# Kernel optimization log

Measured on AMD Instinct MI355X. Metric: run time of the kernel, lower is better.

The kernel has to match this reference:

```python
import jax, jax.numpy as jnp
import numpy as np

OUT = 12                # out_size (cubic grid)
V = OUT * OUT * OUT     # voxels per roi


def setup_inputs() -> dict:
    key = jax.random.key(0)
    k1, k2, k3, k4, k5 = jax.random.split(key, 5)
    N, P, C = 64, 100000, 16
    # rois: (cx, cy, cz_bottom, dx, dy, dz, rz) with sensible LiDAR-scale boxes
    centers = (jax.random.uniform(k1, (N, 3)) - 0.5) * 16.0
    sizes = jax.random.uniform(k2, (N, 3)) * 3.0 + 1.0
    rz = jax.random.uniform(k3, (N, 1)) * np.float32(np.pi)
    rois = jnp.concatenate([centers, sizes, rz], axis=1)
    pts = jax.random.normal(k4, (P, 3)) * 6.0
    pts_feature = jax.random.normal(k5, (P, C))
    return {"rois": rois, "pts": pts, "pts_feature": pts_feature, "mode": 0}


def _pool_one(roi, pts, pts_feature, mode):
    P, C = pts_feature.shape
    cx, cy, cz, dx, dy, dz, rz = roi
    cz = cz + dz * 0.5                      # bottom center -> box center
    sx = pts[:, 0] - cx
    sy = pts[:, 1] - cy
    lz = pts[:, 2] - cz
    cosa = jnp.cos(-rz)
    sina = jnp.sin(-rz)
    lx = sx * cosa - sy * sina              # rotate into roi frame (by -rz)
    ly = sx * sina + sy * cosa
    inbox = (jnp.abs(lz) <= dz * 0.5) & (jnp.abs(lx) < dx * 0.5) & (jnp.abs(ly) < dy * 0.5)
    xi = jnp.clip(jnp.floor((lx + dx * 0.5) / (dx / OUT)).astype(jnp.int32), 0, OUT - 1)
    yi = jnp.clip(jnp.floor((ly + dy * 0.5) / (dy / OUT)).astype(jnp.int32), 0, OUT - 1)
    zi = jnp.clip(jnp.floor((lz + dz * 0.5) / (dz / OUT)).astype(jnp.int32), 0, OUT - 1)
    vid = (xi * OUT + yi) * OUT + zi        # flat voxel id
    seg = jnp.where(inbox, vid, V)          # out-of-box points -> dump segment V
    cnt = jax.ops.segment_sum(jnp.ones((P,), pts_feature.dtype), seg, num_segments=V + 1)[:V]
    if mode == 0:  # max pool: empty voxels stay 0 (as in CUDA kernel init)
        sm = jax.ops.segment_max(pts_feature, seg, num_segments=V + 1)[:V]
        out = jnp.where(cnt[:, None] > 0, sm, jnp.zeros_like(sm))
    else:          # avg pool
        ss = jax.ops.segment_sum(pts_feature, seg, num_segments=V + 1)[:V]
        out = ss / jnp.maximum(cnt[:, None], 1.0)
    return out.reshape(OUT, OUT, OUT, C)


def reference(rois, pts, pts_feature, mode):
    # [N, OUT, OUT, OUT, C]
    return jax.vmap(lambda r: _pool_one(r, pts, pts_feature, mode))(rois)
```

## Files before the change

### kernel.cpp

```cpp
#include <hip/hip_runtime.h>
#include <hip/hip_bf16.h>

#define OUTDIM 12
#define VOX (OUTDIM * OUTDIM * OUTDIM)
#define CS 4
#define BLOCK 512
#define MAXN 256
#define SBLK 256

__device__ __forceinline__ unsigned enc_f32(float f) {
    unsigned u = __float_as_uint(f);
    return (u & 0x80000000u) ? ~u : (u | 0x80000000u);
}
__device__ __forceinline__ float dec_f32(unsigned e) {
    unsigned u = (e & 0x80000000u) ? (e ^ 0x80000000u) : ~e;
    return __uint_as_float(u);
}
__device__ __forceinline__ float bfu2f(unsigned lo16) {
    return __uint_as_float(lo16 << 16);
}
__device__ __forceinline__ unsigned f2bf_bits(float v) {
    __hip_bfloat16 b = __float2bfloat16(v);
    return (unsigned)__builtin_bit_cast(unsigned short, b);
}

__device__ __forceinline__ bool detect_f32(const void* rois_v, int N) {
    const float* rf = (const float*)rois_v;
    int ndet = N / 2; if (ndet > 8) ndet = 8; if (ndet < 1) ndet = 1;
    bool is_f32 = true;
    for (int i = 0; i < ndet; ++i) {
        float a = rf[i * 7 + 3], b = rf[i * 7 + 4], c = rf[i * 7 + 5];
        is_f32 = is_f32 && (a >= 0.99f) && (a <= 4.01f)
                        && (b >= 0.99f) && (b <= 4.01f)
                        && (c >= 0.99f) && (c <= 4.01f);
    }
    return is_f32;
}

__device__ __forceinline__ int decode_mode(const unsigned* mode_p) {
    int mode = 0;
    if (mode_p != nullptr) {
        unsigned u = *mode_p;
        if (u == 1u || u == 0x3f800000u || (u & 0xffffu) == 0x3f80u) mode = 1;
    }
    return mode;
}

struct RoiParams {
    float cx, cy, cz, cosa, sina, hdx, hdy, hdz, stepx, stepy, stepz;
};

__device__ __forceinline__ RoiParams load_roi(const void* rois_v, int n, bool is_f32) {
    float cx, cy, cz, dx, dy, dz, rz;
    if (is_f32) {
        const float* r = (const float*)rois_v + n * 7;
        cx = r[0]; cy = r[1]; cz = r[2];
        dx = r[3]; dy = r[4]; dz = r[5]; rz = r[6];
    } else {
        const ushort* r = (const ushort*)rois_v + n * 7;
        cx = bfu2f(r[0]); cy = bfu2f(r[1]); cz = bfu2f(r[2]);
        dx = bfu2f(r[3]); dy = bfu2f(r[4]); dz = bfu2f(r[5]); rz = bfu2f(r[6]);
    }
    RoiParams rp;
    rp.cx = cx; rp.cy = cy;
    rp.cz = __fadd_rn(cz, __fmul_rn(dz, 0.5f));
    rp.cosa = cosf(-rz);
    rp.sina = sinf(-rz);
    rp.hdx = __fmul_rn(dx, 0.5f);
    rp.hdy = __fmul_rn(dy, 0.5f);
    rp.hdz = __fmul_rn(dz, 0.5f);
    rp.stepx = __fdiv_rn(dx, (float)OUTDIM);
    rp.stepy = __fdiv_rn(dy, (float)OUTDIM);
    rp.stepz = __fdiv_rn(dz, (float)OUTDIM);
    return rp;
}

__device__ __forceinline__ int voxel_of(const RoiParams& rp, float x, float y, float z) {
    float sx = __fsub_rn(x, rp.cx);
    float sy = __fsub_rn(y, rp.cy);
    float lz = __fsub_rn(z, rp.cz);
    float lx = __fsub_rn(__fmul_rn(sx, rp.cosa), __fmul_rn(sy, rp.sina));
    float ly = __fadd_rn(__fmul_rn(sx, rp.sina), __fmul_rn(sy, rp.cosa));
    bool inbox = (fabsf(lz) <= rp.hdz) && (fabsf(lx) < rp.hdx) && (fabsf(ly) < rp.hdy);
    if (!inbox) return -1;
    int xi = (int)floorf(__fdiv_rn(__fadd_rn(lx, rp.hdx), rp.stepx));
    int yi = (int)floorf(__fdiv_rn(__fadd_rn(ly, rp.hdy), rp.stepy));
    int zi = (int)floorf(__fdiv_rn(__fadd_rn(lz, rp.hdz), rp.stepz));
    xi = min(max(xi, 0), OUTDIM - 1);
    yi = min(max(yi, 0), OUTDIM - 1);
    zi = min(max(zi, 0), OUTDIM - 1);
    return (xi * OUTDIM + yi) * OUTDIM + zi;
}

__global__ void __launch_bounds__(SBLK)
roiaware_scatter5(const void* __restrict__ rois_v,
                  const void* __restrict__ pts_v,
                  const void* __restrict__ feat_v,
                  const unsigned* __restrict__ mode_p,
                  unsigned* __restrict__ acc,
                  unsigned* __restrict__ cnt,
                  int P, int N) {
    __shared__ float4 s_a[MAXN];
    __shared__ float4 s_b[MAXN];
    __shared__ float4 s_c[MAXN];

    const int tid = threadIdx.x;
    const bool is_f32 = detect_f32(rois_v, N);
    const int mode = decode_mode(mode_p);

    for (int i = tid; i < N; i += SBLK) {
        RoiParams rp = load_roi(rois_v, i, is_f32);
        s_a[i] = make_float4(rp.cx, rp.cy, rp.cz, rp.cosa);
        s_b[i] = make_float4(rp.sina, rp.hdx, rp.hdy, rp.hdz);
        s_c[i] = make_float4(rp.stepx, rp.stepy, rp.stepz, 0.0f);
    }

    const int p = blockIdx.x * SBLK + tid;
    float x = 1e30f, y = 1e30f, z = 1e30f;
    unsigned vals[16];
    #pragma unroll
    for (int c = 0; c < 16; ++c) vals[c] = 0u;

    if (p < P) {
        if (is_f32) {
            const float* pf = (const float*)pts_v + (size_t)p * 3;
            x = pf[0]; y = pf[1]; z = pf[2];
            const float* f = (const float*)feat_v + (size_t)p * 16;
            #pragma unroll
            for (int c = 0; c < 16; ++c) {
                float v = f[c];
                vals[c] = (mode == 0) ? enc_f32(v) : __float_as_uint(v);
            }
        } else {
            const ushort* pu = (const ushort*)pts_v + (size_t)p * 3;
            x = bfu2f(pu[0]); y = bfu2f(pu[1]); z = bfu2f(pu[2]);
            const ushort* f = (const ushort*)feat_v + (size_t)p * 16;
            uint4 w0 = *(const uint4*)f;
            uint4 w1 = *(const uint4*)(f + 8);
            unsigned w[8] = {w0.x, w0.y, w0.z, w0.w, w1.x, w1.y, w1.z, w1.w};
            #pragma unroll
            for (int k = 0; k < 8; ++k) {
                float v0 = bfu2f(w[k] & 0xffffu);
                float v1 = __uint_as_float(w[k] & 0xffff0000u);
                vals[2 * k]     = (mode == 0) ? enc_f32(v0) : __float_as_uint(v0);
                vals[2 * k + 1] = (mode == 0) ? enc_f32(v1) : __float_as_uint(v1);
            }
        }
    }

    __syncthreads();

    auto do_roi = [&](int j, float4 ra, float4 rb) {
        float sx = __fsub_rn(x, ra.x);
        float sy = __fsub_rn(y, ra.y);
        float lz = __fsub_rn(z, ra.z);
        float lx = __fsub_rn(__fmul_rn(sx, ra.w), __fmul_rn(sy, rb.x));
        float ly = __fadd_rn(__fmul_rn(sx, rb.x), __fmul_rn(sy, ra.w));
        bool inbox = (fabsf(lz) <= rb.w) && (fabsf(lx) < rb.y) && (fabsf(ly) < rb.z);
        if (!inbox) return;

        float4 rc = s_c[j];
        int xi = (int)floorf(__fdiv_rn(__fadd_rn(lx, rb.y), rc.x));
        int yi = (int)floorf(__fdiv_rn(__fadd_rn(ly, rb.z), rc.y));
        int zi = (int)floorf(__fdiv_rn(__fadd_rn(lz, rb.w), rc.z));
        xi = min(max(xi, 0), OUTDIM - 1);
        yi = min(max(yi, 0), OUTDIM - 1);
        zi = min(max(zi, 0), OUTDIM - 1);
        int vid = (xi * OUTDIM + yi) * OUTDIM + zi;

        size_t vbase = (size_t)j * VOX + vid;
        unsigned* a = acc + vbase * 16;
        if (mode == 0) {
            #pragma unroll
            for (int c = 0; c < 16; ++c) atomicMax(&a[c], vals[c]);
        } else {
            atomicAdd(&cnt[vbase], 1u);
            #pragma unroll
            for (int c = 0; c < 16; ++c)
                atomicAdd((float*)&a[c], __uint_as_float(vals[c]));
        }
    };

    int j = 0;
    for (; j + 4 <= N; j += 4) {
        float4 a0 = s_a[j],     b0 = s_b[j];
        float4 a1 = s_a[j + 1], b1 = s_b[j + 1];
        float4 a2 = s_a[j + 2], b2 = s_b[j + 2];
        float4 a3 = s_a[j + 3], b3 = s_b[j + 3];
        do_roi(j,     a0, b0);
        do_roi(j + 1, a1, b1);
        do_roi(j + 2, a2, b2);
        do_roi(j + 3, a3, b3);
    }
    for (; j < N; ++j) do_roi(j, s_a[j], s_b[j]);
}

__global__ void __launch_bounds__(256)
roiaware_finalize3(const void* __restrict__ rois_v,
                   const unsigned* __restrict__ acc,
                   const unsigned* __restrict__ cnt,
                   const unsigned* __restrict__ mode_p,
                   void* __restrict__ out_v,
                   int total_pairs, int N) {
    int i = blockIdx.x * blockDim.x + threadIdx.x;
    if (i >= total_pairs) return;
    const bool is_f32 = detect_f32(rois_v, N);
    const int mode = decode_mode(mode_p);
    uint2 a = *(const uint2*)(acc + (size_t)i * 2);
    float v0, v1;
    if (mode == 0) {
        v0 = a.x ? dec_f32(a.x) : 0.0f;
        v1 = a.y ? dec_f32(a.y) : 0.0f;
    } else {
        unsigned c = cnt[i >> 3];
        float inv = 1.0f / fmaxf((float)c, 1.0f);
        v0 = __uint_as_float(a.x) * inv;
        v1 = __uint_as_float(a.y) * inv;
    }
    if (is_f32) ((float2*)out_v)[i] = make_float2(v0, v1);
    else        ((unsigned*)out_v)[i] = f2bf_bits(v0) | (f2bf_bits(v1) << 16);
}

__global__ void __launch_bounds__(BLOCK)
roiaware_pool(const void* __restrict__ rois_v,
              const void* __restrict__ pts_v,
              const void* __restrict__ feat_v,
              const unsigned* __restrict__ mode_p,
              void* __restrict__ out_v,
              int P, int C, int N) {
    __shared__ unsigned s_acc[VOX * CS];
    __shared__ unsigned s_cnt[VOX];
    const int tid = threadIdx.x;
    const int c0  = blockIdx.x * CS;
    const int n   = blockIdx.y;

    for (int i = tid; i < VOX * CS; i += BLOCK) s_acc[i] = 0u;
    for (int i = tid; i < VOX; i += BLOCK) s_cnt[i] = 0u;

    const bool is_f32 = detect_f32(rois_v, N);
    const int mode = decode_mode(mode_p);
    const RoiParams rp = load_roi(rois_v, n, is_f32);

    const float*  pts_f  = (const float*)pts_v;
    const ushort* pts_u  = (const ushort*)pts_v;
    const float*  feat_f = (const float*)feat_v;
    const ushort* feat_u = (const ushort*)feat_v;

    __syncthreads();

    for (int p = tid; p < P; p += BLOCK) {
        float x, y, z;
        if (is_f32) {
            x = pts_f[p * 3 + 0]; y = pts_f[p * 3 + 1]; z = pts_f[p * 3 + 2];
        } else {
            x = bfu2f(pts_u[p * 3 + 0]);
            y = bfu2f(pts_u[p * 3 + 1]);
            z = bfu2f(pts_u[p * 3 + 2]);
        }
        int vid = voxel_of(rp, x, y, z);
        if (vid < 0) continue;
        atomicAdd(&s_cnt[vid], 1u);
        for (int j = 0; j < CS && (c0 + j) < C; ++j) {
            float fv = is_f32 ? feat_f[(size_t)p * C + c0 + j]
                              : bfu2f(feat_u[(size_t)p * C + c0 + j]);
            unsigned* a = &s_acc[vid * CS + j];
            if (mode == 0) atomicMax(a, enc_f32(fv));
            else           atomicAdd((float*)a, fv);
        }
    }
    __syncthreads();

    for (int i = tid; i < VOX * CS; i += BLOCK) {
        int v = i / CS;
        int j = i % CS;
        if (c0 + j >= C) continue;
        unsigned c = s_cnt[v];
        float val;
        if (mode == 0) val = (c > 0) ? dec_f32(s_acc[i]) : 0.0f;
        else           val = __uint_as_float(s_acc[i]) / fmaxf((float)c, 1.0f);
        size_t oi = ((size_t)n * VOX + v) * C + c0 + j;
        if (is_f32) ((float*)out_v)[oi] = val;
        else        ((__hip_bfloat16*)out_v)[oi] = __float2bfloat16(val);
    }
}

extern "C" void kernel_launch(void* const* d_in, const int* in_sizes, int n_in,
                              void* d_out, int out_size, void* d_ws, size_t ws_size,
                              hipStream_t stream) {
    const void* rois = d_in[0];
    const void* pts  = d_in[1];
    const void* feat = d_in[2];
    const unsigned* mode_p = nullptr;
    if (n_in >= 4 && in_sizes[3] >= 1 && d_in[3] != nullptr) {
        mode_p = (const unsigned*)d_in[3];
    }

    int N = in_sizes[0] / 7;
    int P = in_sizes[1] / 3;
    int C = in_sizes[2] / P;

    size_t need = ((size_t)N * VOX * C + (size_t)N * VOX) * sizeof(unsigned);

    if (C == 16 && N <= MAXN && ws_size >= need) {
        unsigned* acc = (unsigned*)d_ws;
        unsigned* cnt = acc + (size_t)N * VOX * 16;
        (void)hipMemsetAsync(d_ws, 0, need, stream);

        roiaware_scatter5<<<(P + SBLK - 1) / SBLK, SBLK, 0, stream>>>(
            rois, pts, feat, mode_p, acc, cnt, P, N);

        int total_pairs = N * VOX * 8;
        roiaware_finalize3<<<(total_pairs + 255) / 256, 256, 0, stream>>>(
            rois, acc, cnt, mode_p, d_out, total_pairs, N);
    } else {
        dim3 grid((C + CS - 1) / CS, N);
        roiaware_pool<<<grid, BLOCK, 0, stream>>>(rois, pts, feat, mode_p,
                                                  d_out, P, C, N);
    }
}
```

Before: 88.22 us.

## Add bounding-sphere prefilter with per-point ROI bitmask in scatter kernel

Each point first runs a cheap squared-distance test against a bounding sphere for every ROI and records the candidates in a 64-bit mask. It then runs the full rotated box test and voxel/atomic path only for those candidates. The block size is reduced to 64 threads, one wavefront, and the fast path is limited to at most 64 ROIs. This is meant to replace per-ROI divergent box tests with a uniform filter plus sparse iteration. The cost is that larger N falls back to the slow kernel, and the smaller blocks reload the ROI table more often.

```diff
diff --git a/kernel.cpp b/kernel.cpp
--- a/kernel.cpp
+++ b/kernel.cpp
@@ -5,8 +5,7 @@
 #define VOX (OUTDIM * OUTDIM * OUTDIM)
 #define CS 4
 #define BLOCK 512
-#define MAXN 256
-#define SBLK 256
+#define SBLK 64
 
 __device__ __forceinline__ unsigned enc_f32(float f) {
     unsigned u = __float_as_uint(f);
@@ -93,29 +92,32 @@
 }
 
 __global__ void __launch_bounds__(SBLK)
-roiaware_scatter5(const void* __restrict__ rois_v,
+roiaware_scatter7(const void* __restrict__ rois_v,
                   const void* __restrict__ pts_v,
                   const void* __restrict__ feat_v,
                   const unsigned* __restrict__ mode_p,
                   unsigned* __restrict__ acc,
                   unsigned* __restrict__ cnt,
                   int P, int N) {
-    __shared__ float4 s_a[MAXN];
-    __shared__ float4 s_b[MAXN];
-    __shared__ float4 s_c[MAXN];
-
-    const int tid = threadIdx.x;
+    __shared__ float4 s_s[64];
+    __shared__ float4 s_a[64];
+    __shared__ float4 s_b[64];
+    __shared__ float4 s_c[64];
+
+    const int lane = threadIdx.x;
     const bool is_f32 = detect_f32(rois_v, N);
     const int mode = decode_mode(mode_p);
 
-    for (int i = tid; i < N; i += SBLK) {
-        RoiParams rp = load_roi(rois_v, i, is_f32);
-        s_a[i] = make_float4(rp.cx, rp.cy, rp.cz, rp.cosa);
-        s_b[i] = make_float4(rp.sina, rp.hdx, rp.hdy, rp.hdz);
-        s_c[i] = make_float4(rp.stepx, rp.stepy, rp.stepz, 0.0f);
-    }
-
-    const int p = blockIdx.x * SBLK + tid;
+    if (lane < N) {
+        RoiParams rp = load_roi(rois_v, lane, is_f32);
+        float r2 = rp.hdx * rp.hdx + rp.hdy * rp.hdy + rp.hdz * rp.hdz;
+        s_s[lane] = make_float4(rp.cx, rp.cy, rp.cz, r2 * 1.001f);
+        s_a[lane] = make_float4(rp.cx, rp.cy, rp.cz, rp.cosa);
+        s_b[lane] = make_float4(rp.sina, rp.hdx, rp.hdy, rp.hdz);
+        s_c[lane] = make_float4(rp.stepx, rp.stepy, rp.stepz, 0.0f);
+    }
+
+    const int p = blockIdx.x * SBLK + lane;
     float x = 1e30f, y = 1e30f, z = 1e30f;
     unsigned vals[16];
     #pragma unroll
@@ -150,16 +152,42 @@
 
     __syncthreads();
 
-    auto do_roi = [&](int j, float4 ra, float4 rb) {
+    unsigned long long mask = 0ull;
+    auto sph = [&](int j) -> unsigned long long {
+        float4 s = s_s[j];
+        float dx = x - s.x, dy = y - s.y, dz = z - s.z;
+        float d2 = fmaf(dx, dx, fmaf(dy, dy, dz * dz));
+        return (d2 <= s.w) ? (1ull << j) : 0ull;
+    };
+    int j = 0;
+    for (; j + 4 <= N; j += 4) {
+        float4 s0 = s_s[j], s1 = s_s[j + 1], s2 = s_s[j + 2], s3 = s_s[j + 3];
+        float d0 = fmaf(x - s0.x, x - s0.x, fmaf(y - s0.y, y - s0.y, (z - s0.z) * (z - s0.z)));
+        float d1 = fmaf(x - s1.x, x - s1.x, fmaf(y - s1.y, y - s1.y, (z - s1.z) * (z - s1.z)));
+        float d2_ = fmaf(x - s2.x, x - s2.x, fmaf(y - s2.y, y - s2.y, (z - s2.z) * (z - s2.z)));
+        float d3 = fmaf(x - s3.x, x - s3.x, fmaf(y - s3.y, y - s3.y, (z - s3.z) * (z - s3.z)));
+        if (d0 <= s0.w) mask |= 1ull << j;
+        if (d1 <= s1.w) mask |= 1ull << (j + 1);
+        if (d2_ <= s2.w) mask |= 1ull << (j + 2);
+        if (d3 <= s3.w) mask |= 1ull << (j + 3);
+    }
+    for (; j < N; ++j) mask |= sph(j);
+
+    while (mask) {
+        int jj = __ffsll((unsigned long long)mask) - 1;
+        mask &= mask - 1;
+
+        float4 ra = s_a[jj];
+        float4 rb = s_b[jj];
         float sx = __fsub_rn(x, ra.x);
         float sy = __fsub_rn(y, ra.y);
         float lz = __fsub_rn(z, ra.z);
         float lx = __fsub_rn(__fmul_rn(sx, ra.w), __fmul_rn(sy, rb.x));
         float ly = __fadd_rn(__fmul_rn(sx, rb.x), __fmul_rn(sy, ra.w));
         bool inbox = (fabsf(lz) <= rb.w) && (fabsf(lx) < rb.y) && (fabsf(ly) < rb.z);
-        if (!inbox) return;
-
-        float4 rc = s_c[j];
+        if (!inbox) continue;
+
+        float4 rc = s_c[jj];
         int xi = (int)floorf(__fdiv_rn(__fadd_rn(lx, rb.y), rc.x));
         int yi = (int)floorf(__fdiv_rn(__fadd_rn(ly, rb.z), rc.y));
         int zi = (int)floorf(__fdiv_rn(__fadd_rn(lz, rb.w), rc.z));
@@ -168,7 +196,7 @@
         zi = min(max(zi, 0), OUTDIM - 1);
         int vid = (xi * OUTDIM + yi) * OUTDIM + zi;
 
-        size_t vbase = (size_t)j * VOX + vid;
+        size_t vbase = (size_t)jj * VOX + vid;
         unsigned* a = acc + vbase * 16;
         if (mode == 0) {
             #pragma unroll
@@ -179,20 +207,7 @@
             for (int c = 0; c < 16; ++c)
                 atomicAdd((float*)&a[c], __uint_as_float(vals[c]));
         }
-    };
-
-    int j = 0;
-    for (; j + 4 <= N; j += 4) {
-        float4 a0 = s_a[j],     b0 = s_b[j];
-        float4 a1 = s_a[j + 1], b1 = s_b[j + 1];
-        float4 a2 = s_a[j + 2], b2 = s_b[j + 2];
-        float4 a3 = s_a[j + 3], b3 = s_b[j + 3];
-        do_roi(j,     a0, b0);
-        do_roi(j + 1, a1, b1);
-        do_roi(j + 2, a2, b2);
-        do_roi(j + 3, a3, b3);
-    }
-    for (; j < N; ++j) do_roi(j, s_a[j], s_b[j]);
+    }
 }
 
 __global__ void __launch_bounds__(256)
@@ -301,12 +316,12 @@
 
     size_t need = ((size_t)N * VOX * C + (size_t)N * VOX) * sizeof(unsigned);
 
-    if (C == 16 && N <= MAXN && ws_size >= need) {
+    if (C == 16 && N <= 64 && ws_size >= need) {
         unsigned* acc = (unsigned*)d_ws;
         unsigned* cnt = acc + (size_t)N * VOX * 16;
         (void)hipMemsetAsync(d_ws, 0, need, stream);
 
-        roiaware_scatter5<<<(P + SBLK - 1) / SBLK, SBLK, 0, stream>>>(
+        roiaware_scatter7<<<(P + SBLK - 1) / SBLK, SBLK, 0, stream>>>(
             rois, pts, feat, mode_p, acc, cnt, P, N);
 
         int total_pairs = N * VOX * 8;
```

New measurement: 87.76 us. No clear change (-0.5%).
